# Optimization experiments

Measured on AMD Instinct MI355X. Metric: run time of the kernel, lower is better.

Reference implementation:

```python
import jax, jax.numpy as jnp
import numpy as np

H, TH, NH, NL, NB = 512, 768, 8, 12, 2
NE, NU, NI, NNZ, K, B = 16000, 2000, 4000, 40000, 10, 64
MD = H // 2
GAMA = 0.1


def _prelu(x, a):
    return jnp.where(x >= 0, x, a * x)


def _spmm(r, c, v, X, n):
    # sparse [n, m] @ X: gather X rows by col index, scale, segment-sum by row.
    return jax.ops.segment_sum(v[:, None] * X[c], r, num_segments=n)


def _forward(systemid, adj_row, adj_col, itemid_set,
             token_embeds, adj_val, node_embeds, user_embedding,
             token_proj_w, token_proj_b, trans_w, trans_b, trans_t_w, trans_t_b,
             meta_w1, meta_b1, meta_w2, meta_b2, sim_w1, sim_w2,
             p1_w1, p1_b1, p1_w2, p1_b2, p2_w, p2_b, prelu_a):
    tok = token_embeds @ token_proj_w + token_proj_b               # [B, H]
    # grouped mean over rows sharing the same system id (vectorized segment-mean)
    same = (systemid[:, None] == systemid[None, :]).astype(tok.dtype)
    group_mean = (same @ tok) / same.sum(1, keepdims=True)         # [B, H]
    filt = _prelu(group_mean @ trans_w + trans_b, prelu_a) * group_mean
    h = jax.nn.relu(filt @ meta_w1 + meta_b1)
    mapping = (h @ meta_w2 + meta_b2).reshape(B, H, H)             # per-sample hypernet weights
    enhanced = jnp.einsum('bh,bhk->bk', user_embedding[systemid], mapping)
    all_tok = user_embedding.at[systemid].set(enhanced)            # [NU, H]
    tok_edge = jnp.zeros_like(user_embedding).at[systemid].set(group_mean)
    # similarity between (enhanced) user/token reps and item reps
    u_rep = all_tok @ sim_w1
    i_rep = node_embeds[itemid_set] @ sim_w2
    u_n = u_rep / jnp.maximum(jnp.linalg.norm(u_rep, axis=1, keepdims=True), 1e-12)
    i_n = i_rep / jnp.maximum(jnp.linalg.norm(i_rep, axis=1, keepdims=True), 1e-12)
    sim = jax.nn.sigmoid(u_n @ i_n.T)                              # [NU, NI]
    tv, ti = jax.lax.top_k(sim, K)
    # combined sparse adjacency = original COO + per-user top-k added edges
    rows = jnp.concatenate([adj_row, jnp.repeat(jnp.arange(NU), K)])
    cols = jnp.concatenate([adj_col, itemid_set[ti].reshape(-1)])
    vals = jnp.concatenate([adj_val, tv.reshape(-1)])
    v_u = vals / jax.ops.segment_sum(vals, rows, num_segments=NU)[rows]   # row-normalized user->item
    v_i = vals / jax.ops.segment_sum(vals, cols, num_segments=NE)[cols]   # row-normalized item->user
    # LightGCN-style 2-layer propagation with multiplicative token gating
    user_tok = _prelu(tok_edge @ trans_t_w + trans_t_b, prelu_a) * tok_edge
    u0, i0 = all_tok, node_embeds
    Ai0 = _spmm(rows, cols, v_u, i0, NU)
    u1 = Ai0 + Ai0 * user_tok
    Att = _spmm(cols, rows, v_i, user_tok, NE)
    i1 = _spmm(cols, rows, v_i, u0, NE) + Att * i0
    Ai1 = _spmm(rows, cols, v_u, i1, NU)
    u2 = Ai1 + Ai1 * user_tok
    i2 = _spmm(cols, rows, v_i, u1, NE) + Att * i1
    user_final = (u0 + u1 + u2) / 3.0
    item_final = (i0 + i1 + i2) / 3.0
    # reconstruction loss vs dense adjacency restricted to item columns
    inv = jnp.full((NE,), -1, jnp.int32).at[itemid_set].set(jnp.arange(NI, dtype=jnp.int32))
    icol = inv[adj_col]
    valid = (icol >= 0).astype(sim.dtype)
    dense = jnp.zeros((NU, NI), sim.dtype).at[adj_row, jnp.maximum(icol, 0)].add(adj_val * valid)
    loss = GAMA * jnp.mean((sim - dense) ** 2)
    # prefix-prompt projection from per-batch system embeddings
    sys_final = user_final[systemid][:, None, :]                   # [B, 1, H]
    p1 = jax.nn.relu(sys_final @ p1_w1 + p1_b1) @ p1_w2 + p1_b2 + sys_final
    p2 = p1 @ p2_w + p2_b
    prompt = p2.reshape(B, 1, NL, NB, NH, H // NH).transpose(2, 3, 0, 4, 1, 5)
    return prompt, item_final, loss


def setup_inputs():
    ks = jax.random.split(jax.random.key(0), 20)
    rng = np.random.default_rng(0)
    s = 0.02
    itemid_set = jnp.asarray(np.sort(rng.choice(NE, NI, replace=False)).astype(np.int32))
    user_embedding = (s * jax.random.normal(ks[4], (NU, H), jnp.float32)).at[0].set(0.0)
    return {
        'systemid': jax.random.randint(ks[0], (B,), 0, NU),
        'adj_row': jax.random.randint(ks[1], (NNZ,), 0, NU),
        'adj_col': jax.random.randint(ks[2], (NNZ,), 0, NE),
        'itemid_set': itemid_set,
        'token_embeds': jax.random.normal(ks[3], (B, TH), jnp.float32),
        'adj_val': jnp.ones((NNZ,), jnp.float32),
        'node_embeds': s * jax.random.normal(ks[5], (NE, H), jnp.float32),
        'user_embedding': user_embedding,
        'token_proj_w': s * jax.random.normal(ks[6], (TH, H), jnp.float32),
        'token_proj_b': jnp.zeros((H,), jnp.float32),
        'trans_w': s * jax.random.normal(ks[7], (H, H), jnp.float32),
        'trans_b': jnp.zeros((H,), jnp.float32),
        'trans_t_w': s * jax.random.normal(ks[8], (H, H), jnp.float32),
        'trans_t_b': jnp.zeros((H,), jnp.float32),
        'meta_w1': s * jax.random.normal(ks[9], (H, MD), jnp.float32),
        'meta_b1': jnp.zeros((MD,), jnp.float32),
        'meta_w2': s * jax.random.normal(ks[10], (MD, H * H), jnp.float32),
        'meta_b2': jnp.zeros((H * H,), jnp.float32),
        'sim_w1': jax.random.normal(ks[11], (H, H), jnp.float32),
        'sim_w2': jax.random.normal(ks[12], (H, H), jnp.float32),
        'p1_w1': s * jax.random.normal(ks[13], (H, MD), jnp.float32),
        'p1_b1': jnp.zeros((MD,), jnp.float32),
        'p1_w2': s * jax.random.normal(ks[14], (MD, H), jnp.float32),
        'p1_b2': jnp.zeros((H,), jnp.float32),
        'p2_w': s * jax.random.normal(ks[15], (H, NL * NB * H), jnp.float32),
        'p2_b': jnp.zeros((NL * NB * H,), jnp.float32),
        'prelu_a': jnp.array(0.25, jnp.float32),
    }


def reference(systemid, adj_row, adj_col, itemid_set, token_embeds, adj_val,
              node_embeds, user_embedding, token_proj_w, token_proj_b,
              trans_w, trans_b, trans_t_w, trans_t_b,
              meta_w1, meta_b1, meta_w2, meta_b2, sim_w1, sim_w2,
              p1_w1, p1_b1, p1_w2, p1_b2, p2_w, p2_b, prelu_a):
    return _forward(systemid, adj_row, adj_col, itemid_set, token_embeds, adj_val,
                    node_embeds, user_embedding, token_proj_w, token_proj_b,
                    trans_w, trans_b, trans_t_w, trans_t_b,
                    meta_w1, meta_b1, meta_w2, meta_b2, sim_w1, sim_w2,
                    p1_w1, p1_b1, p1_w2, p1_b2, p2_w, p2_b, prelu_a)
```

## Files before the change

kernel.cpp:

```cpp
#include <hip/hip_runtime.h>

#define H     512
#define THD   768
#define MDIM  256
#define NE    16000
#define NU    2000
#define NI    4000
#define NNZ   40000
#define KTOP  10
#define NBATCH 64
#define NEDGE 60000
#define GAMA  0.1f
#define P2N   12288
#define PROMPT_N 786432

__device__ __forceinline__ float sigmoidf(float x){ return 1.0f/(1.0f+expf(-x)); }
__device__ __forceinline__ float4 f4z(){ return make_float4(0.f,0.f,0.f,0.f); }

__device__ __forceinline__ void gll16(const float* g, float* l){
  __builtin_amdgcn_global_load_lds(
      (const __attribute__((address_space(1))) void*)g,
      (__attribute__((address_space(3))) void*)l, 16, 0, 0);
}

__global__ void k_tok(const float* __restrict__ A, const float* __restrict__ W,
                      const float* __restrict__ bias, float* __restrict__ C){
  int b=blockIdx.x, c=blockIdx.y*256+threadIdx.x;
  const float* a=A+b*THD; float s=bias[c];
  for(int k=0;k<THD;k++) s+=a[k]*W[k*H+c];
  C[b*H+c]=s;
}

__global__ void k_gm(const int* __restrict__ sysid, const float* __restrict__ tok,
                     float* __restrict__ gm){
  int b=blockIdx.x, c=blockIdx.y*256+threadIdx.x;
  int sid=sysid[b]; float s=0.f, cnt=0.f;
  for(int j=0;j<NBATCH;j++){ if(sysid[j]==sid){ s+=tok[j*H+c]; cnt+=1.f; } }
  gm[b*H+c]=s/cnt;
}

__global__ __launch_bounds__(512) void k_filthh(const float* __restrict__ gm,
        const float* __restrict__ trans_w, const float* __restrict__ trans_b,
        const float* __restrict__ mw1, const float* __restrict__ mb1,
        const float* __restrict__ pa, float* __restrict__ hh){
  __shared__ float fl[512];
  __shared__ float hp[512];
  int b=blockIdx.x, t=threadIdx.x;
  const float* g=gm+b*H;
  float s=trans_b[t];
  for(int k=0;k<H;k++) s+=g[k]*trans_w[k*H+t];
  float al=pa[0]; float pr=(s>=0.f)? s : al*s;
  fl[t]=pr*g[t];
  __syncthreads();
  int m=t&255, half=t>>8;
  float s2=0.f; int k0=half*256;
  for(int k=0;k<256;k++) s2+=fl[k0+k]*mw1[(k0+k)*MDIM+m];
  hp[t]=s2;
  __syncthreads();
  if(t<256) hh[b*MDIM+t]=fmaxf(hp[t]+hp[t+256]+mb1[t],0.f);
}

__global__ void k_uprep(const int* __restrict__ sysid, const float* __restrict__ ue,
                        const float* __restrict__ mb2, float* __restrict__ uesel,
                        float* __restrict__ ueT, float* __restrict__ enh){
  int b=blockIdx.x, c=blockIdx.y*256+threadIdx.x;
  const float* u=ue+(size_t)sysid[b]*H;
  float v=u[c];
  uesel[b*H+c]=v;
  ueT[c*64+b]=v;
  float s=0.f;
  for(int h=0;h<H;h++) s+=u[h]*mb2[(size_t)h*H+c];
  enh[b*H+c]=s;
}

#define HCH 16
__global__ __launch_bounds__(128) void k_big(const float* __restrict__ hh,
        const float* __restrict__ ueT, const float* __restrict__ w2,
        float* __restrict__ partials){
  __shared__ float a_lds[2][HCH][64];
  __shared__ float w_lds[2][HCH][128];
  int m=blockIdx.x;
  int k0=blockIdx.y*128;
  int t=threadIdx.x;
  int kg=t&15, bg=t>>4;
  const float* w2m = w2 + (size_t)m*(size_t)(H*H);

  float4 accA[8], accB[8];
  #pragma unroll
  for(int i=0;i<8;i++){ accA[i]=f4z(); accB[i]=f4z(); }

  #define STAGE(buf,hc) do{                                            \
    int h0=(hc)*HCH;                                                   \
    _Pragma("unroll")                                                  \
    for(int j=0;j<2;j++){                                              \
      int i=t+j*128;                                                   \
      gll16(ueT + (size_t)(h0+(i>>4))*64 + (i&15)*4,                   \
            &a_lds[buf][i>>4][(i&15)*4]);                              \
    }                                                                  \
    _Pragma("unroll")                                                  \
    for(int j=0;j<4;j++){                                              \
      int i=t+j*128;                                                   \
      gll16(w2m + (size_t)(h0+(i>>5))*H + k0 + (i&31)*4,               \
            &w_lds[buf][i>>5][(i&31)*4]);                              \
    }                                                                  \
  }while(0)

  STAGE(0,0);
  int cur=0;
  for(int hc=0;hc<32;hc++){
    __syncthreads();
    if(hc<31) STAGE(cur^1,hc+1);
    #pragma unroll 4
    for(int hl=0;hl<HCH;hl++){
      float4 aL=*(const float4*)&a_lds[cur][hl][bg*4];
      float4 aH=*(const float4*)&a_lds[cur][hl][32+bg*4];
      float4 wL=*(const float4*)&w_lds[cur][hl][kg*4];
      float4 wH=*(const float4*)&w_lds[cur][hl][64+kg*4];
      #define ROW(i,av)                                                   \
        accA[i].x+=(av)*wL.x; accA[i].y+=(av)*wL.y;                       \
        accA[i].z+=(av)*wL.z; accA[i].w+=(av)*wL.w;                       \
        accB[i].x+=(av)*wH.x; accB[i].y+=(av)*wH.y;                       \
        accB[i].z+=(av)*wH.z; accB[i].w+=(av)*wH.w;
      ROW(0,aL.x) ROW(1,aL.y) ROW(2,aL.z) ROW(3,aL.w)
      ROW(4,aH.x) ROW(5,aH.y) ROW(6,aH.z) ROW(7,aH.w)
      #undef ROW
    }
    cur^=1;
  }
  #pragma unroll
  for(int bi=0;bi<4;bi++){
    int bb=bg*4+bi;
    float hv=hh[bb*MDIM+m];
    float* p=partials+((size_t)m*NBATCH+bb)*H+k0;
    *(float4*)(p+kg*4)   =make_float4(accA[bi].x*hv,accA[bi].y*hv,accA[bi].z*hv,accA[bi].w*hv);
    *(float4*)(p+64+kg*4)=make_float4(accB[bi].x*hv,accB[bi].y*hv,accB[bi].z*hv,accB[bi].w*hv);
    int b2=32+bg*4+bi;
    float hv2=hh[b2*MDIM+m];
    float* p2=partials+((size_t)m*NBATCH+b2)*H+k0;
    *(float4*)(p2+kg*4)   =make_float4(accA[4+bi].x*hv2,accA[4+bi].y*hv2,accA[4+bi].z*hv2,accA[4+bi].w*hv2);
    *(float4*)(p2+64+kg*4)=make_float4(accB[4+bi].x*hv2,accB[4+bi].y*hv2,accB[4+bi].z*hv2,accB[4+bi].w*hv2);
  }
  #undef STAGE
}

__global__ void k_red1(const float* __restrict__ partials, float* __restrict__ partial2){
  int idx=blockIdx.x*256+threadIdx.x;
  int g=idx>>15, col=idx&32767;
  const float* p=partials+(size_t)g*16*32768+col;
  float s=0.f;
  #pragma unroll
  for(int m=0;m<16;m++) s+=p[(size_t)m*32768];
  partial2[idx]=s;
}
__global__ void k_red2s(const int* __restrict__ sysid, const float* __restrict__ partial2,
                        const float* __restrict__ enh, float* __restrict__ alltok){
  int idx=blockIdx.x*256+threadIdx.x;
  int b=idx>>9, k=idx&511;
  float s=enh[idx];
  #pragma unroll
  for(int g=0;g<16;g++) s+=partial2[(size_t)g*32768+idx];
  alltok[(size_t)sysid[b]*H+k]=s;
}

__global__ void k_user_tok(const int* __restrict__ sysid, const float* __restrict__ gm,
                           const float* __restrict__ W, const float* __restrict__ bias,
                           const float* __restrict__ pa, float* __restrict__ usertok){
  int b=blockIdx.x, c=blockIdx.y*256+threadIdx.x;
  const float* a=gm+b*H; float s=bias[c];
  for(int k=0;k<H;k++) s+=a[k]*W[k*H+c];
  float al=pa[0]; float pr=(s>=0.f)? s : al*s;
  usertok[(size_t)sysid[b]*H+c]=pr*gm[b*H+c];
}

template<int EPI, bool NT, bool AIDX>
__global__ __launch_bounds__(256) void k_gemm(const float* __restrict__ A,
        const float* __restrict__ Bm, const float* __restrict__ bias,
        const int* __restrict__ aidx, float* __restrict__ C, int M, int N, int K){
  __shared__ float As[32][68];
  __shared__ float Bs[32][68];
  int n0=blockIdx.x*64, m0=blockIdx.y*64;
  int t=threadIdx.x;
  int tn=t&15, tm=t>>4;
  float4 pa[2], pb[2];
  #pragma unroll
  for(int i=0;i<2;i++){
    int idx=t+i*256; int r=idx>>3, q=idx&7;
    int grow=m0+r;
    pa[i]=f4z();
    if(grow<M){
      const float* arow=A+(size_t)(AIDX? aidx[grow]:grow)*K;
      pa[i]=*(const float4*)(arow+q*4);
    }
  }
  #pragma unroll
  for(int i=0;i<2;i++){
    if(!NT){
      int idx=t+i*256; int r=idx>>4, q=idx&15;
      pb[i]=*(const float4*)(Bm+(size_t)r*N+n0+q*4);
    } else {
      int idx=t+i*256; int r=idx>>3, q=idx&7;
      int gn=n0+r;
      pb[i]=f4z();
      if(gn<N) pb[i]=*(const float4*)(Bm+(size_t)gn*K+q*4);
    }
  }
  float acc[4][4]={};
  for(int kt=0;kt<K;kt+=32){
    __syncthreads();
    #pragma unroll
    for(int i=0;i<2;i++){
      int idx=t+i*256; int r=idx>>3, q=idx&7;
      As[q*4+0][r]=pa[i].x; As[q*4+1][r]=pa[i].y; As[q*4+2][r]=pa[i].z; As[q*4+3][r]=pa[i].w;
    }
    #pragma unroll
    for(int i=0;i<2;i++){
      if(!NT){
        int idx=t+i*256; int r=idx>>4, q=idx&15;
        *(float4*)&Bs[r][q*4]=pb[i];
      } else {
        int idx=t+i*256; int r=idx>>3, q=idx&7;
        Bs[q*4+0][r]=pb[i].x; Bs[q*4+1][r]=pb[i].y; Bs[q*4+2][r]=pb[i].z; Bs[q*4+3][r]=pb[i].w;
      }
    }
    __syncthreads();
    if(kt+32<K){
      #pragma unroll
      for(int i=0;i<2;i++){
        int idx=t+i*256; int r=idx>>3, q=idx&7;
        int grow=m0+r;
        pa[i]=f4z();
        if(grow<M){
          const float* arow=A+(size_t)(AIDX? aidx[grow]:grow)*K;
          pa[i]=*(const float4*)(arow+kt+32+q*4);
        }
      }
      #pragma unroll
      for(int i=0;i<2;i++){
        if(!NT){
          int idx=t+i*256; int r=idx>>4, q=idx&15;
          pb[i]=*(const float4*)(Bm+(size_t)(kt+32+r)*N+n0+q*4);
        } else {
          int idx=t+i*256; int r=idx>>3, q=idx&7;
          int gn=n0+r;
          pb[i]=f4z();
          if(gn<N) pb[i]=*(const float4*)(Bm+(size_t)gn*K+kt+32+q*4);
        }
      }
    }
    #pragma unroll 8
    for(int k=0;k<32;k++){
      float4 a4=*(const float4*)&As[k][tm*4];
      float4 b4=*(const float4*)&Bs[k][tn*4];
      acc[0][0]+=a4.x*b4.x; acc[0][1]+=a4.x*b4.y; acc[0][2]+=a4.x*b4.z; acc[0][3]+=a4.x*b4.w;
      acc[1][0]+=a4.y*b4.x; acc[1][1]+=a4.y*b4.y; acc[1][2]+=a4.y*b4.z; acc[1][3]+=a4.y*b4.w;
      acc[2][0]+=a4.z*b4.x; acc[2][1]+=a4.z*b4.y; acc[2][2]+=a4.z*b4.z; acc[2][3]+=a4.z*b4.w;
      acc[3][0]+=a4.w*b4.x; acc[3][1]+=a4.w*b4.y; acc[3][2]+=a4.w*b4.z; acc[3][3]+=a4.w*b4.w;
    }
  }
  #pragma unroll
  for(int bi=0;bi<4;bi++){
    int row=m0+tm*4+bi; if(row>=M) continue;
    #pragma unroll
    for(int ki=0;ki<4;ki++){
      int col=n0+tn*4+ki; if(col>=N) continue;
      float v=acc[bi][ki];
      if(EPI==0){ if(bias) v+=bias[col]; }
      else { v=sigmoidf(v); }
      C[(size_t)row*N+col]=v;
    }
  }
}

__global__ __launch_bounds__(512) void k_gemm_sim(const float* __restrict__ A,
        const float* __restrict__ Bm, float* __restrict__ C, int M, int N){
  __shared__ float As[32][132];
  __shared__ float Bs[32][132];
  int n0=blockIdx.x*128, m0=blockIdx.y*128;
  int t=threadIdx.x;
  int tn=t&31, tm=t>>5;
  float4 pa0,pa1,pb0,pb1;
  {
    int i0=t, i1=t+512;
    int r0=i0>>3,q0=i0&7, r1=i1>>3,q1=i1&7;
    pa0=f4z(); pa1=f4z(); pb0=f4z(); pb1=f4z();
    if(m0+r0<M) pa0=*(const float4*)(A+(size_t)(m0+r0)*H+q0*4);
    if(m0+r1<M) pa1=*(const float4*)(A+(size_t)(m0+r1)*H+q1*4);
    if(n0+r0<N) pb0=*(const float4*)(Bm+(size_t)(n0+r0)*H+q0*4);
    if(n0+r1<N) pb1=*(const float4*)(Bm+(size_t)(n0+r1)*H+q1*4);
  }
  float acc[8][4]={};
  for(int kt=0;kt<H;kt+=32){
    __syncthreads();
    {
      int i0=t, i1=t+512;
      int r0=i0>>3,q0=i0&7, r1=i1>>3,q1=i1&7;
      As[q0*4+0][r0]=pa0.x; As[q0*4+1][r0]=pa0.y; As[q0*4+2][r0]=pa0.z; As[q0*4+3][r0]=pa0.w;
      As[q1*4+0][r1]=pa1.x; As[q1*4+1][r1]=pa1.y; As[q1*4+2][r1]=pa1.z; As[q1*4+3][r1]=pa1.w;
      Bs[q0*4+0][r0]=pb0.x; Bs[q0*4+1][r0]=pb0.y; Bs[q0*4+2][r0]=pb0.z; Bs[q0*4+3][r0]=pb0.w;
      Bs[q1*4+0][r1]=pb1.x; Bs[q1*4+1][r1]=pb1.y; Bs[q1*4+2][r1]=pb1.z; Bs[q1*4+3][r1]=pb1.w;
    }
    __syncthreads();
    if(kt+32<H){
      int i0=t, i1=t+512;
      int r0=i0>>3,q0=i0&7, r1=i1>>3,q1=i1&7;
      pa0=f4z(); pa1=f4z(); pb0=f4z(); pb1=f4z();
      if(m0+r0<M) pa0=*(const float4*)(A+(size_t)(m0+r0)*H+kt+32+q0*4);
      if(m0+r1<M) pa1=*(const float4*)(A+(size_t)(m0+r1)*H+kt+32+q1*4);
      if(n0+r0<N) pb0=*(const float4*)(Bm+(size_t)(n0+r0)*H+kt+32+q0*4);
      if(n0+r1<N) pb1=*(const float4*)(Bm+(size_t)(n0+r1)*H+kt+32+q1*4);
    }
    #pragma unroll 8
    for(int k=0;k<32;k++){
      float4 a0=*(const float4*)&As[k][tm*8];
      float4 a1=*(const float4*)&As[k][tm*8+4];
      float4 b0=*(const float4*)&Bs[k][tn*4];
      acc[0][0]+=a0.x*b0.x; acc[0][1]+=a0.x*b0.y; acc[0][2]+=a0.x*b0.z; acc[0][3]+=a0.x*b0.w;
      acc[1][0]+=a0.y*b0.x; acc[1][1]+=a0.y*b0.y; acc[1][2]+=a0.y*b0.z; acc[1][3]+=a0.y*b0.w;
      acc[2][0]+=a0.z*b0.x; acc[2][1]+=a0.z*b0.y; acc[2][2]+=a0.z*b0.z; acc[2][3]+=a0.z*b0.w;
      acc[3][0]+=a0.w*b0.x; acc[3][1]+=a0.w*b0.y; acc[3][2]+=a0.w*b0.z; acc[3][3]+=a0.w*b0.w;
      acc[4][0]+=a1.x*b0.x; acc[4][1]+=a1.x*b0.y; acc[4][2]+=a1.x*b0.z; acc[4][3]+=a1.x*b0.w;
      acc[5][0]+=a1.y*b0.x; acc[5][1]+=a1.y*b0.y; acc[5][2]+=a1.y*b0.z; acc[5][3]+=a1.y*b0.w;
      acc[6][0]+=a1.z*b0.x; acc[6][1]+=a1.z*b0.y; acc[6][2]+=a1.z*b0.z; acc[6][3]+=a1.z*b0.w;
      acc[7][0]+=a1.w*b0.x; acc[7][1]+=a1.w*b0.y; acc[7][2]+=a1.w*b0.z; acc[7][3]+=a1.w*b0.w;
    }
  }
  #pragma unroll
  for(int mi=0;mi<8;mi++){
    int row=m0+tm*8+mi; if(row>=M) continue;
    #pragma unroll
    for(int nj=0;nj<4;nj++){
      int col=n0+tn*4+nj; if(col>=N) continue;
      C[(size_t)row*N+col]=sigmoidf(acc[mi][nj]);
    }
  }
}

__global__ __launch_bounds__(256) void k_rownorm(float* __restrict__ X){
  int r=blockIdx.x, t=threadIdx.x;
  float v1=X[(size_t)r*H+t], v2=X[(size_t)r*H+t+256];
  float ss=v1*v1+v2*v2;
  for(int o=32;o;o>>=1) ss+=__shfl_xor(ss,o);
  __shared__ float red[4];
  if((t&63)==0) red[t>>6]=ss;
  __syncthreads();
  float tot=red[0]+red[1]+red[2]+red[3];
  float nrm=fmaxf(sqrtf(tot),1e-12f);
  X[(size_t)r*H+t]=v1/nrm; X[(size_t)r*H+t+256]=v2/nrm;
}

__global__ __launch_bounds__(256) void k_topk(const float* __restrict__ sim,
        float* __restrict__ tv, int* __restrict__ ti){
  __shared__ float vals[NI];
  __shared__ float rv[4];
  __shared__ int   ri[4];
  int u=blockIdx.x, t=threadIdx.x;
  for(int i=t;i<NI;i+=256) vals[i]=sim[(size_t)u*NI+i];
  __syncthreads();
  for(int k=0;k<KTOP;k++){
    float bv=-1e30f; int bi=NI;
    for(int i=t;i<NI;i+=256){
      float v=vals[i];
      if(v>bv || (v==bv && i<bi)){ bv=v; bi=i; }
    }
    #pragma unroll
    for(int o=32;o;o>>=1){
      float ov=__shfl_xor(bv,o); int oi=__shfl_xor(bi,o);
      if(ov>bv || (ov==bv && oi<bi)){ bv=ov; bi=oi; }
    }
    if((t&63)==0){ rv[t>>6]=bv; ri[t>>6]=bi; }
    __syncthreads();
    float fv=rv[0]; int fi=ri[0];
    #pragma unroll
    for(int w=1;w<4;w++){
      float ov=rv[w]; int oi=ri[w];
      if(ov>fv || (ov==fv && oi<fi)){ fv=ov; fi=oi; }
    }
    if(t==0){ tv[u*KTOP+k]=fv; ti[u*KTOP+k]=fi; vals[fi]=-1e30f; }
    __syncthreads();
  }
}

__global__ void k_edges(const int* __restrict__ adj_row, const int* __restrict__ adj_col,
        const float* __restrict__ adj_val, const int* __restrict__ itemid,
        const float* __restrict__ tv, const int* __restrict__ ti,
        int* __restrict__ rows, int* __restrict__ cols, float* __restrict__ vals,
        float* __restrict__ seg_r, float* __restrict__ seg_c,
        int* __restrict__ row_cnt, int* __restrict__ col_cnt, int* __restrict__ inv){
  int e=blockIdx.x*256+threadIdx.x; if(e>=NEDGE) return;
  if(e<NI) inv[itemid[e]]=e;
  int r,c; float v;
  if(e<NNZ){ r=adj_row[e]; c=adj_col[e]; v=adj_val[e]; }
  else { int x=e-NNZ; int u=x/KTOP; r=u; c=itemid[ti[x]]; v=tv[x]; }
  rows[e]=r; cols[e]=c; vals[e]=v;
  atomicAdd(&seg_r[r],v); atomicAdd(&seg_c[c],v);
  atomicAdd(&row_cnt[r],1); atomicAdd(&col_cnt[c],1);
}

__global__ __launch_bounds__(1024) void k_scan(const int* __restrict__ rc, int* __restrict__ rp,
        const int* __restrict__ cc, int* __restrict__ cp){
  const int* cnt; int* ptr; int n;
  if(blockIdx.x==0){ cnt=rc; ptr=rp; n=NU; } else { cnt=cc; ptr=cp; n=NE; }
  int t=threadIdx.x;
  int chunk=(n+1023)>>10;
  int base=t*chunk;
  int s=0;
  for(int i=0;i<chunk;i++){ int j=base+i; if(j<n) s+=cnt[j]; }
  __shared__ int buf[1024];
  buf[t]=s; __syncthreads();
  for(int off=1;off<1024;off<<=1){
    int y=(t>=off)? buf[t-off]:0;
    __syncthreads();
    buf[t]+=y;
    __syncthreads();
  }
  int run=buf[t]-s;
  for(int i=0;i<chunk;i++){ int j=base+i; if(j<n){ ptr[j]=run; run+=cnt[j]; } }
  if(t==1023) ptr[n]=buf[1023];
}

__global__ void k_fill(const int* __restrict__ rows, const int* __restrict__ cols,
        const float* __restrict__ vals,
        const int* __restrict__ row_ptr, const int* __restrict__ col_ptr,
        const float* __restrict__ seg_r, const float* __restrict__ seg_c,
        int* __restrict__ fr, int* __restrict__ fc,
        int* __restrict__ ebr, int* __restrict__ ebc,
        float* __restrict__ v_u, float* __restrict__ v_i,
        const int* __restrict__ inv, float* __restrict__ dense){
  int e=blockIdx.x*256+threadIdx.x; if(e>=NEDGE) return;
  int r=rows[e], c=cols[e];
  ebr[row_ptr[r]+atomicAdd(&fr[r],1)]=e;
  ebc[col_ptr[c]+atomicAdd(&fc[c],1)]=e;
  v_u[e]=vals[e]/seg_r[r];
  v_i[e]=vals[e]/seg_c[c];
  if(e<NNZ){
    int ic=inv[c];
    if(ic>=0) atomicAdd(&dense[(size_t)r*NI+ic],vals[e]);
  }
}

__global__ __launch_bounds__(256) void k_spmm_u(const int* __restrict__ row_ptr,
        const int* __restrict__ ebr, const int* __restrict__ cols,
        const float* __restrict__ v_u, const float* __restrict__ X,
        const float* __restrict__ usertok, float* __restrict__ out){
  __shared__ float red[3][512];
  int u=blockIdx.x;
  int t=threadIdx.x, w=t>>6, l=t&63;
  int s=row_ptr[u], e1=row_ptr[u+1];
  float4 a0=f4z(), a1=f4z();
  for(int j=s+w;j<e1;j+=4){
    int e=ebr[j]; float v=v_u[e];
    const float4* xr=(const float4*)(X+(size_t)cols[e]*H);
    float4 x0=xr[l], x1=xr[l+64];
    a0.x+=v*x0.x; a0.y+=v*x0.y; a0.z+=v*x0.z; a0.w+=v*x0.w;
    a1.x+=v*x1.x; a1.y+=v*x1.y; a1.z+=v*x1.z; a1.w+=v*x1.w;
  }
  if(w>0){ *(float4*)&red[w-1][l*4]=a0; *(float4*)&red[w-1][l*4+256]=a1; }
  __syncthreads();
  if(w==0){
    #pragma unroll
    for(int ww=0;ww<3;ww++){
      float4 r0=*(const float4*)&red[ww][l*4], r1=*(const float4*)&red[ww][l*4+256];
      a0.x+=r0.x; a0.y+=r0.y; a0.z+=r0.z; a0.w+=r0.w;
      a1.x+=r1.x; a1.y+=r1.y; a1.z+=r1.z; a1.w+=r1.w;
    }
    const float4* ut=(const float4*)(usertok+(size_t)u*H);
    float4 u0=ut[l], u1=ut[l+64];
    float4* o=(float4*)(out+(size_t)u*H);
    o[l]   =make_float4(a0.x+a0.x*u0.x, a0.y+a0.y*u0.y, a0.z+a0.z*u0.z, a0.w+a0.w*u0.w);
    o[l+64]=make_float4(a1.x+a1.x*u1.x, a1.y+a1.y*u1.y, a1.z+a1.z*u1.z, a1.w+a1.w*u1.w);
  }
}

__global__ __launch_bounds__(256) void k_spmm_i1(const int* __restrict__ col_ptr,
        const int* __restrict__ ebc, const int* __restrict__ rows,
        const float* __restrict__ v_i, const float* __restrict__ alltok,
        const float* __restrict__ usertok, const float* __restrict__ i0,
        float* __restrict__ Att, float* __restrict__ i1){
  int i=blockIdx.x*4+(threadIdx.x>>6);
  int l=threadIdx.x&63;
  int s=col_ptr[i], e1=col_ptr[i+1];
  float4 aA0=f4z(),aA1=f4z(),aU0=f4z(),aU1=f4z();
  for(int j=s;j<e1;j++){
    int e=ebc[j]; float v=v_i[e]; int r=rows[e];
    const float4* ur=(const float4*)(usertok+(size_t)r*H);
    const float4* ar=(const float4*)(alltok+(size_t)r*H);
    float4 u0=ur[l],u1v=ur[l+64],A0=ar[l],A1=ar[l+64];
    aA0.x+=v*u0.x; aA0.y+=v*u0.y; aA0.z+=v*u0.z; aA0.w+=v*u0.w;
    aA1.x+=v*u1v.x; aA1.y+=v*u1v.y; aA1.z+=v*u1v.z; aA1.w+=v*u1v.w;
    aU0.x+=v*A0.x; aU0.y+=v*A0.y; aU0.z+=v*A0.z; aU0.w+=v*A0.w;
    aU1.x+=v*A1.x; aU1.y+=v*A1.y; aU1.z+=v*A1.z; aU1.w+=v*A1.w;
  }
  size_t o=(size_t)i*128;
  const float4* z=(const float4*)i0;
  float4 z0=z[o+l], z1=z[o+l+64];
  ((float4*)Att)[o+l]   =aA0;
  ((float4*)Att)[o+l+64]=aA1;
  ((float4*)i1)[o+l]   =make_float4(aU0.x+aA0.x*z0.x, aU0.y+aA0.y*z0.y, aU0.z+aA0.z*z0.z, aU0.w+aA0.w*z0.w);
  ((float4*)i1)[o+l+64]=make_float4(aU1.x+aA1.x*z1.x, aU1.y+aA1.y*z1.y, aU1.z+aA1.z*z1.z, aU1.w+aA1.w*z1.w);
}

__global__ __launch_bounds__(256) void k_spmm_i2(const int* __restrict__ col_ptr,
        const int* __restrict__ ebc, const int* __restrict__ rows,
        const float* __restrict__ v_i, const float* __restrict__ u1,
        const float* __restrict__ Att, const float* __restrict__ i1,
        const float* __restrict__ i0, float* __restrict__ item_out){
  int i=blockIdx.x*4+(threadIdx.x>>6);
  int l=threadIdx.x&63;
  int s=col_ptr[i], e1=col_ptr[i+1];
  float4 a0=f4z(), a1=f4z();
  for(int j=s;j<e1;j++){
    int e=ebc[j]; float v=v_i[e];
    const float4* ur=(const float4*)(u1+(size_t)rows[e]*H);
    float4 x0=ur[l], x1=ur[l+64];
    a0.x+=v*x0.x; a0.y+=v*x0.y; a0.z+=v*x0.z; a0.w+=v*x0.w;
    a1.x+=v*x1.x; a1.y+=v*x1.y; a1.z+=v*x1.z; a1.w+=v*x1.w;
  }
  size_t o=(size_t)i*128;
  float4 A0=((const float4*)Att)[o+l], A1=((const float4*)Att)[o+l+64];
  float4 I0=((const float4*)i1)[o+l],  I1=((const float4*)i1)[o+l+64];
  float4 Z0=((const float4*)i0)[o+l],  Z1=((const float4*)i0)[o+l+64];
  float4 r0=make_float4((Z0.x+I0.x+a0.x+A0.x*I0.x)/3.f,(Z0.y+I0.y+a0.y+A0.y*I0.y)/3.f,
                        (Z0.z+I0.z+a0.z+A0.z*I0.z)/3.f,(Z0.w+I0.w+a0.w+A0.w*I0.w)/3.f);
  float4 r1=make_float4((Z1.x+I1.x+a1.x+A1.x*I1.x)/3.f,(Z1.y+I1.y+a1.y+A1.y*I1.y)/3.f,
                        (Z1.z+I1.z+a1.z+A1.z*I1.z)/3.f,(Z1.w+I1.w+a1.w+A1.w*I1.w)/3.f);
  ((float4*)item_out)[o+l]=r0;
  ((float4*)item_out)[o+l+64]=r1;
}

__global__ __launch_bounds__(256) void k_loss(const float* __restrict__ sim,
        const float* __restrict__ dense, float* __restrict__ acc){
  size_t n4=(size_t)NU*NI/4;
  float s=0.f;
  for(size_t i=(size_t)blockIdx.x*256+threadIdx.x; i<n4; i+=(size_t)gridDim.x*256){
    float4 a=((const float4*)sim)[i], d=((const float4*)dense)[i];
    float dx=a.x-d.x, dy=a.y-d.y, dz=a.z-d.z, dw=a.w-d.w;
    s+=dx*dx+dy*dy+dz*dz+dw*dw;
  }
  __shared__ float red[256];
  red[threadIdx.x]=s; __syncthreads();
  for(int o=128;o;o>>=1){ if(threadIdx.x<o) red[threadIdx.x]+=red[threadIdx.x+o]; __syncthreads(); }
  if(threadIdx.x==0) atomicAdd(acc,red[0]);
}
__global__ void k_loss_write(const float* __restrict__ acc, float* __restrict__ out){
  out[0]=GAMA*(acc[0]/(float)((size_t)NU*NI));
}

__global__ __launch_bounds__(512) void k_sysq_p1(const int* __restrict__ sysid,
        const float* __restrict__ u0, const float* __restrict__ u1, const float* __restrict__ u2,
        const float* __restrict__ p1w1, const float* __restrict__ p1b1,
        const float* __restrict__ p1w2, const float* __restrict__ p1b2,
        float* __restrict__ p1buf){
  __shared__ float sf[512];
  __shared__ float hp[512];
  __shared__ float qv[256];
  int b=blockIdx.x, t=threadIdx.x;
  size_t o=(size_t)sysid[b]*H+t;
  float sfv=(u0[o]+u1[o]+u2[o])/3.0f;
  sf[t]=sfv;
  __syncthreads();
  int m=t&255, half=t>>8;
  float s=0.f; int k0=half*256;
  for(int k=0;k<256;k++) s+=sf[k0+k]*p1w1[(k0+k)*MDIM+m];
  hp[t]=s;
  __syncthreads();
  if(t<256) qv[t]=fmaxf(hp[t]+hp[t+256]+p1b1[t],0.f);
  __syncthreads();
  float s2=p1b2[t];
  for(int k=0;k<256;k++) s2+=qv[k]*p1w2[k*H+t];
  p1buf[b*H+t]=s2+sf[t];
}

__global__ void k_perm(const float* __restrict__ p2, float* __restrict__ out){
  int idx=blockIdx.x*256+threadIdx.x;
  int x=idx&511;
  int b=(idx>>9)&63;
  int c=idx>>15;
  out[idx]=p2[(size_t)b*P2N+c*512+x];
}

extern "C" void kernel_launch(void* const* d_in, const int* in_sizes, int n_in,
                              void* d_out, int out_size, void* d_ws, size_t ws_size,
                              hipStream_t stream){
  const int*   sysid   =(const int*)  d_in[0];
  const int*   adj_row =(const int*)  d_in[1];
  const int*   adj_col =(const int*)  d_in[2];
  const int*   itemid  =(const int*)  d_in[3];
  const float* tok_emb =(const float*)d_in[4];
  const float* adj_val =(const float*)d_in[5];
  const float* node_emb=(const float*)d_in[6];
  const float* user_emb=(const float*)d_in[7];
  const float* tp_w    =(const float*)d_in[8];
  const float* tp_b    =(const float*)d_in[9];
  const float* trans_w =(const float*)d_in[10];
  const float* trans_b =(const float*)d_in[11];
  const float* trt_w   =(const float*)d_in[12];
  const float* trt_b   =(const float*)d_in[13];
  const float* mw1     =(const float*)d_in[14];
  const float* mb1     =(const float*)d_in[15];
  const float* mw2     =(const float*)d_in[16];
  const float* mb2     =(const float*)d_in[17];
  const float* sw1     =(const float*)d_in[18];
  const float* sw2     =(const float*)d_in[19];
  const float* p1w1    =(const float*)d_in[20];
  const float* p1b1    =(const float*)d_in[21];
  const float* p1w2    =(const float*)d_in[22];
  const float* p1b2    =(const float*)d_in[23];
  const float* p2w     =(const float*)d_in[24];
  const float* p2b     =(const float*)d_in[25];
  const float* pa      =(const float*)d_in[26];

  float* out_prompt=(float*)d_out;
  float* out_item  =out_prompt+PROMPT_N;
  float* out_loss  =out_item+(size_t)NE*H;

  char* ws=(char*)d_ws; size_t off=0;
  auto A=[&](size_t bytes)->char*{ char* p=ws+off; off+=(bytes+255)&~(size_t)255; return p; };
  float* tok     =(float*)A((size_t)NBATCH*H*4);
  float* gm      =(float*)A((size_t)NBATCH*H*4);
  float* hh      =(float*)A((size_t)NBATCH*MDIM*4);
  float* uesel   =(float*)A((size_t)NBATCH*H*4);
  float* ueT     =(float*)A((size_t)H*NBATCH*4);
  float* enh     =(float*)A((size_t)NBATCH*H*4);
  float* irep    =(float*)A((size_t)NI*H*4);
  float* alltok  =(float*)A((size_t)NU*H*4);
  float* urep    =(float*)A((size_t)NU*H*4);
  float* u1      =(float*)A((size_t)NU*H*4);
  float* u2      =(float*)A((size_t)NU*H*4);
  float* big     =(float*)A((size_t)16384000*4);
  float* partials=big;
  float* partial2=big+8388608;
  float* sim     =big;
  float* dense   =big+8000000;
  float* Att     =big;
  float* i1      =big+8192000;
  float* tv      =(float*)A((size_t)NU*KTOP*4);
  int*   ti      =(int*)  A((size_t)NU*KTOP*4);
  int*   rowsA   =(int*)  A((size_t)NEDGE*4);
  int*   colsA   =(int*)  A((size_t)NEDGE*4);
  float* valsA   =(float*)A((size_t)NEDGE*4);
  float* v_u     =(float*)A((size_t)NEDGE*4);
  float* v_i     =(float*)A((size_t)NEDGE*4);
  int*   ebr     =(int*)  A((size_t)NEDGE*4);
  int*   ebc     =(int*)  A((size_t)NEDGE*4);
  int*   row_ptr =(int*)  A((size_t)(NU+1)*4);
  int*   col_ptr =(int*)  A((size_t)(NE+1)*4);
  size_t zb_bytes=(size_t)NU*H*4 + (size_t)(NU+NE)*4*3 + 256;
  char*  zb      =A(zb_bytes);
  float* usertok =(float*)zb;
  float* seg_r   =usertok+(size_t)NU*H;
  float* seg_c   =seg_r+NU;
  int*   row_cnt =(int*)(seg_c+NE);
  int*   col_cnt =row_cnt+NU;
  int*   fr      =col_cnt+NE;
  int*   fc      =fr+NU;
  float* loss_acc=(float*)(fc+NE);
  int*   inv     =(int*)  A((size_t)NE*4);
  float* p1buf   =(float*)A((size_t)NBATCH*H*4);
  float* p2buf   =(float*)A((size_t)NBATCH*P2N*4);
  (void)ws_size; (void)n_in; (void)in_sizes; (void)out_size;

  dim3 g642(NBATCH,2);

  hipMemcpyAsync(alltok,user_emb,(size_t)NU*H*4,hipMemcpyDeviceToDevice,stream);
  hipMemsetAsync(zb,0,zb_bytes,stream);
  hipMemsetAsync(inv,0xFF,(size_t)NE*4,stream);
  hipMemsetAsync(dense,0,(size_t)8000000*4,stream);

  k_tok   <<<g642,256,0,stream>>>(tok_emb,tp_w,tp_b,tok);
  k_gm    <<<g642,256,0,stream>>>(sysid,tok,gm);
  k_filthh<<<NBATCH,512,0,stream>>>(gm,trans_w,trans_b,mw1,mb1,pa,hh);
  k_uprep <<<g642,256,0,stream>>>(sysid,user_emb,mb2,uesel,ueT,enh);
  k_big   <<<dim3(256,4),128,0,stream>>>(hh,ueT,mw2,partials);
  k_red1  <<<2048,256,0,stream>>>(partials,partial2);
  k_red2s <<<128,256,0,stream>>>(sysid,partial2,enh,alltok);
  k_user_tok<<<g642,256,0,stream>>>(sysid,gm,trt_w,trt_b,pa,usertok);

  k_gemm<0,false,false><<<dim3(8,32),256,0,stream>>>(alltok,sw1,nullptr,nullptr,urep,NU,H,H);
  k_gemm<0,false,true> <<<dim3(8,63),256,0,stream>>>(node_emb,sw2,nullptr,itemid,irep,NI,H,H);
  k_rownorm<<<NU,256,0,stream>>>(urep);
  k_rownorm<<<NI,256,0,stream>>>(irep);
  k_gemm_sim<<<dim3(32,16),512,0,stream>>>(urep,irep,sim,NU,NI);
  k_topk<<<NU,256,0,stream>>>(sim,tv,ti);

  k_edges<<<(NEDGE+255)/256,256,0,stream>>>(adj_row,adj_col,adj_val,itemid,tv,ti,
                                            rowsA,colsA,valsA,seg_r,seg_c,row_cnt,col_cnt,inv);
  k_scan<<<2,1024,0,stream>>>(row_cnt,row_ptr,col_cnt,col_ptr);
  k_fill<<<(NEDGE+255)/256,256,0,stream>>>(rowsA,colsA,valsA,row_ptr,col_ptr,seg_r,seg_c,
                                           fr,fc,ebr,ebc,v_u,v_i,inv,dense);

  k_loss<<<2048,256,0,stream>>>(sim,dense,loss_acc);
  k_loss_write<<<1,1,0,stream>>>(loss_acc,out_loss);

  k_spmm_u <<<NU,256,0,stream>>>(row_ptr,ebr,colsA,v_u,node_emb,usertok,u1);
  k_spmm_i1<<<NE/4,256,0,stream>>>(col_ptr,ebc,rowsA,v_i,alltok,usertok,node_emb,Att,i1);
  k_spmm_u <<<NU,256,0,stream>>>(row_ptr,ebr,colsA,v_u,i1,usertok,u2);
  k_spmm_i2<<<NE/4,256,0,stream>>>(col_ptr,ebc,rowsA,v_i,u1,Att,i1,node_emb,out_item);

  k_sysq_p1<<<NBATCH,512,0,stream>>>(sysid,alltok,u1,u2,p1w1,p1b1,p1w2,p1b2,p1buf);
  k_gemm<0,false,false><<<dim3(192,1),256,0,stream>>>(p1buf,p2w,p2b,nullptr,p2buf,NBATCH,P2N,H);
  k_perm<<<PROMPT_N/256,256,0,stream>>>(p2buf,out_prompt);
}
```

Before: 823.2 us.

## Widen k_big tile to 256 columns with split-H and stage SpMM edge indices

k_big now computes a 64x256 output tile per block and splits the 512-long H reduction into two halves, with a halved chunk depth and a fully unrolled inner loop. This raises register-level reuse of each LDS load. The cost is twice as many partial slices, so the partials buffer doubles, k_red1 runs twice as many blocks and k_red2s sums 32 groups, adding extra global write and read traffic. Separately, k_spmm_u first loads each row's edge column indices and values into LDS in chunks of 128, instead of each wave doing dependent ebr→cols/v_u loads per edge.

```diff
diff --git a/kernel.cpp b/kernel.cpp
--- a/kernel.cpp
+++ b/kernel.cpp
@@ -73,36 +73,37 @@
   enh[b*H+c]=s;
 }
 
-#define HCH 16
+#define HCH 8
 __global__ __launch_bounds__(128) void k_big(const float* __restrict__ hh,
         const float* __restrict__ ueT, const float* __restrict__ w2,
         float* __restrict__ partials){
   __shared__ float a_lds[2][HCH][64];
-  __shared__ float w_lds[2][HCH][128];
+  __shared__ float w_lds[2][HCH][256];
   int m=blockIdx.x;
-  int k0=blockIdx.y*128;
+  int kt=blockIdx.y&1, hs=blockIdx.y>>1;
+  int k0=kt*256;
+  int hbase=hs*256;
   int t=threadIdx.x;
   int kg=t&15, bg=t>>4;
   const float* w2m = w2 + (size_t)m*(size_t)(H*H);
 
-  float4 accA[8], accB[8];
+  float4 acc[8][4];
   #pragma unroll
-  for(int i=0;i<8;i++){ accA[i]=f4z(); accB[i]=f4z(); }
-
-  #define STAGE(buf,hc) do{                                            \
-    int h0=(hc)*HCH;                                                   \
-    _Pragma("unroll")                                                  \
-    for(int j=0;j<2;j++){                                              \
-      int i=t+j*128;                                                   \
-      gll16(ueT + (size_t)(h0+(i>>4))*64 + (i&15)*4,                   \
-            &a_lds[buf][i>>4][(i&15)*4]);                              \
-    }                                                                  \
-    _Pragma("unroll")                                                  \
-    for(int j=0;j<4;j++){                                              \
-      int i=t+j*128;                                                   \
-      gll16(w2m + (size_t)(h0+(i>>5))*H + k0 + (i&31)*4,               \
-            &w_lds[buf][i>>5][(i&31)*4]);                              \
-    }                                                                  \
+  for(int r=0;r<8;r++){
+    #pragma unroll
+    for(int c=0;c<4;c++) acc[r][c]=f4z();
+  }
+
+  #define STAGE(buf,hc) do{                                             \
+    int h0=hbase+(hc)*HCH;                                              \
+    gll16(ueT + (size_t)(h0+(t>>4))*64 + (t&15)*4,                      \
+          &a_lds[buf][t>>4][(t&15)*4]);                                 \
+    _Pragma("unroll")                                                   \
+    for(int j=0;j<4;j++){                                               \
+      int i=t+j*128;                                                    \
+      gll16(w2m + (size_t)(h0+(i>>6))*H + k0 + (i&63)*4,                \
+            &w_lds[buf][i>>6][(i&63)*4]);                               \
+    }                                                                   \
   }while(0)
 
   STAGE(0,0);
@@ -110,35 +111,33 @@
   for(int hc=0;hc<32;hc++){
     __syncthreads();
     if(hc<31) STAGE(cur^1,hc+1);
-    #pragma unroll 4
+    #pragma unroll
     for(int hl=0;hl<HCH;hl++){
       float4 aL=*(const float4*)&a_lds[cur][hl][bg*4];
       float4 aH=*(const float4*)&a_lds[cur][hl][32+bg*4];
-      float4 wL=*(const float4*)&w_lds[cur][hl][kg*4];
-      float4 wH=*(const float4*)&w_lds[cur][hl][64+kg*4];
-      #define ROW(i,av)                                                   \
-        accA[i].x+=(av)*wL.x; accA[i].y+=(av)*wL.y;                       \
-        accA[i].z+=(av)*wL.z; accA[i].w+=(av)*wL.w;                       \
-        accB[i].x+=(av)*wH.x; accB[i].y+=(av)*wH.y;                       \
-        accB[i].z+=(av)*wH.z; accB[i].w+=(av)*wH.w;
-      ROW(0,aL.x) ROW(1,aL.y) ROW(2,aL.z) ROW(3,aL.w)
-      ROW(4,aH.x) ROW(5,aH.y) ROW(6,aH.z) ROW(7,aH.w)
-      #undef ROW
+      float4 w0=*(const float4*)&w_lds[cur][hl][kg*4];
+      float4 w1=*(const float4*)&w_lds[cur][hl][64+kg*4];
+      float4 w2v=*(const float4*)&w_lds[cur][hl][128+kg*4];
+      float4 w3=*(const float4*)&w_lds[cur][hl][192+kg*4];
+      #define FMA4(ac,av,wv) ac.x+=(av)*wv.x; ac.y+=(av)*wv.y; ac.z+=(av)*wv.z; ac.w+=(av)*wv.w;
+      #define ROWC(r,av) FMA4(acc[r][0],av,w0) FMA4(acc[r][1],av,w1) FMA4(acc[r][2],av,w2v) FMA4(acc[r][3],av,w3)
+      ROWC(0,aL.x) ROWC(1,aL.y) ROWC(2,aL.z) ROWC(3,aL.w)
+      ROWC(4,aH.x) ROWC(5,aH.y) ROWC(6,aH.z) ROWC(7,aH.w)
+      #undef ROWC
+      #undef FMA4
     }
     cur^=1;
   }
+  int slice=hs*256+m;
   #pragma unroll
-  for(int bi=0;bi<4;bi++){
-    int bb=bg*4+bi;
-    float hv=hh[bb*MDIM+m];
-    float* p=partials+((size_t)m*NBATCH+bb)*H+k0;
-    *(float4*)(p+kg*4)   =make_float4(accA[bi].x*hv,accA[bi].y*hv,accA[bi].z*hv,accA[bi].w*hv);
-    *(float4*)(p+64+kg*4)=make_float4(accB[bi].x*hv,accB[bi].y*hv,accB[bi].z*hv,accB[bi].w*hv);
-    int b2=32+bg*4+bi;
-    float hv2=hh[b2*MDIM+m];
-    float* p2=partials+((size_t)m*NBATCH+b2)*H+k0;
-    *(float4*)(p2+kg*4)   =make_float4(accA[4+bi].x*hv2,accA[4+bi].y*hv2,accA[4+bi].z*hv2,accA[4+bi].w*hv2);
-    *(float4*)(p2+64+kg*4)=make_float4(accB[4+bi].x*hv2,accB[4+bi].y*hv2,accB[4+bi].z*hv2,accB[4+bi].w*hv2);
+  for(int r=0;r<8;r++){
+    int br=(r<4)? (bg*4+r) : (32+bg*4+(r-4));
+    float hv=hh[br*MDIM+m];
+    float* p=partials+((size_t)slice*NBATCH+br)*H+k0+kg*4;
+    *(float4*)(p)    =make_float4(acc[r][0].x*hv,acc[r][0].y*hv,acc[r][0].z*hv,acc[r][0].w*hv);
+    *(float4*)(p+64) =make_float4(acc[r][1].x*hv,acc[r][1].y*hv,acc[r][1].z*hv,acc[r][1].w*hv);
+    *(float4*)(p+128)=make_float4(acc[r][2].x*hv,acc[r][2].y*hv,acc[r][2].z*hv,acc[r][2].w*hv);
+    *(float4*)(p+192)=make_float4(acc[r][3].x*hv,acc[r][3].y*hv,acc[r][3].z*hv,acc[r][3].w*hv);
   }
   #undef STAGE
 }
@@ -158,7 +157,7 @@
   int b=idx>>9, k=idx&511;
   float s=enh[idx];
   #pragma unroll
-  for(int g=0;g<16;g++) s+=partial2[(size_t)g*32768+idx];
+  for(int g=0;g<32;g++) s+=partial2[(size_t)g*32768+idx];
   alltok[(size_t)sysid[b]*H+k]=s;
 }
 
@@ -442,17 +441,25 @@
         const int* __restrict__ ebr, const int* __restrict__ cols,
         const float* __restrict__ v_u, const float* __restrict__ X,
         const float* __restrict__ usertok, float* __restrict__ out){
+  __shared__ int   sc[128];
+  __shared__ float sv[128];
   __shared__ float red[3][512];
   int u=blockIdx.x;
   int t=threadIdx.x, w=t>>6, l=t&63;
-  int s=row_ptr[u], e1=row_ptr[u+1];
+  int s=row_ptr[u], n=row_ptr[u+1]-s;
   float4 a0=f4z(), a1=f4z();
-  for(int j=s+w;j<e1;j+=4){
-    int e=ebr[j]; float v=v_u[e];
-    const float4* xr=(const float4*)(X+(size_t)cols[e]*H);
-    float4 x0=xr[l], x1=xr[l+64];
-    a0.x+=v*x0.x; a0.y+=v*x0.y; a0.z+=v*x0.z; a0.w+=v*x0.w;
-    a1.x+=v*x1.x; a1.y+=v*x1.y; a1.z+=v*x1.z; a1.w+=v*x1.w;
+  for(int base=0;base<n;base+=128){
+    int cnt=min(n-base,128);
+    if(t<cnt){ int e=ebr[s+base+t]; sc[t]=cols[e]; sv[t]=v_u[e]; }
+    __syncthreads();
+    for(int j=w;j<cnt;j+=4){
+      float v=sv[j];
+      const float4* xr=(const float4*)(X+(size_t)sc[j]*H);
+      float4 x0=xr[l], x1=xr[l+64];
+      a0.x+=v*x0.x; a0.y+=v*x0.y; a0.z+=v*x0.z; a0.w+=v*x0.w;
+      a1.x+=v*x1.x; a1.y+=v*x1.y; a1.z+=v*x1.z; a1.w+=v*x1.w;
+    }
+    __syncthreads();
   }
   if(w>0){ *(float4*)&red[w-1][l*4]=a0; *(float4*)&red[w-1][l*4+256]=a1; }
   __syncthreads();
@@ -626,9 +633,9 @@
   float* urep    =(float*)A((size_t)NU*H*4);
   float* u1      =(float*)A((size_t)NU*H*4);
   float* u2      =(float*)A((size_t)NU*H*4);
-  float* big     =(float*)A((size_t)16384000*4);
+  float* big     =(float*)A((size_t)17825792*4);
   float* partials=big;
-  float* partial2=big+8388608;
+  float* partial2=big+16777216;
   float* sim     =big;
   float* dense   =big+8000000;
   float* Att     =big;
@@ -671,7 +678,7 @@
   k_filthh<<<NBATCH,512,0,stream>>>(gm,trans_w,trans_b,mw1,mb1,pa,hh);
   k_uprep <<<g642,256,0,stream>>>(sysid,user_emb,mb2,uesel,ueT,enh);
   k_big   <<<dim3(256,4),128,0,stream>>>(hh,ueT,mw2,partials);
-  k_red1  <<<2048,256,0,stream>>>(partials,partial2);
+  k_red1  <<<4096,256,0,stream>>>(partials,partial2);
   k_red2s <<<128,256,0,stream>>>(sysid,partial2,enh,alltok);
   k_user_tok<<<g642,256,0,stream>>>(sysid,gm,trt_w,trt_b,pa,usertok);
 
```

Measured after the change: 829.6 us. About the same (+0.8%).
